# Kernel optimization log

Hardware: AMD Instinct MI355X
Metric: run time of the kernel (lower is better)

The kernel has to match this reference:

```python
import jax, jax.numpy as jnp
import numpy as np

B, S, D_MODEL, N_HEADS = 4, 2048, 1024, 16
HEAD_DIM = D_MODEL // N_HEADS  # 64; used only for the softmax scale, as in the source


def setup_inputs() -> dict:
    key = jax.random.key(0)
    kq, kk, kv, kw = jax.random.split(key, 4)
    q = jax.random.normal(kq, (B, S, D_MODEL), dtype=jnp.float32)
    k = jax.random.normal(kk, (B, S, D_MODEL), dtype=jnp.float32)
    v = jax.random.normal(kv, (B, S, D_MODEL), dtype=jnp.float32)
    # out_proj: nn.Linear(d_model, d_model, bias=False) -> weight [out, in]
    W_out = jax.random.normal(kw, (D_MODEL, D_MODEL), dtype=jnp.float32) * (1.0 / np.sqrt(D_MODEL))
    return {"q": q, "k": k, "v": v, "W_out": W_out}


def reference(q, k, v, W_out):
    scale = 1.0 / jnp.sqrt(jnp.float32(HEAD_DIM))
    # scores: [B, Sq, Sk] -- full quadratic score matrix, as in the source
    scores = jnp.einsum("bqd,bkd->bqk", q, k) * scale
    attn = jax.nn.softmax(scores, axis=-1)
    out = jnp.einsum("bqk,bkd->bqd", attn, v)
    # torch Linear: y = x @ W^T
    return jnp.einsum("bsd,ed->bse", out, W_out)
```

## Files before the change

kernel.cpp:

```cpp
#include <hip/hip_runtime.h>
#include <hip/hip_fp16.h>
#include <stdint.h>

typedef _Float16 h16;
typedef _Float16 h16x8 __attribute__((ext_vector_type(8)));
typedef float f32x4 __attribute__((ext_vector_type(4)));

#define BB 4
#define SS 2048
#define DD 1024

__device__ __forceinline__ void gload16(const void* g, void* l) {
    __builtin_amdgcn_global_load_lds(
        (const __attribute__((address_space(1))) uint32_t*)g,
        (__attribute__((address_space(3))) uint32_t*)l, 16, 0, 0);
}

__global__ __launch_bounds__(256) void cvt_f32_h16(const float* __restrict__ in,
                                                   h16* __restrict__ out,
                                                   int n8, float scale) {
    int i = blockIdx.x * 256 + threadIdx.x;
    if (i >= n8) return;
    const float4* p = (const float4*)in + (size_t)i * 2;
    float4 a = p[0], b = p[1];
    union { int4 i4; h16 h[8]; } u;
    u.h[0] = (h16)(a.x * scale); u.h[1] = (h16)(a.y * scale);
    u.h[2] = (h16)(a.z * scale); u.h[3] = (h16)(a.w * scale);
    u.h[4] = (h16)(b.x * scale); u.h[5] = (h16)(b.y * scale);
    u.h[6] = (h16)(b.z * scale); u.h[7] = (h16)(b.w * scale);
    ((int4*)out)[i] = u.i4;
}

template<int BM, bool F32OUT>
__global__ __launch_bounds__(512, 2) void gemm8p(
    const h16* __restrict__ A, const h16* __restrict__ B, void* __restrict__ Cv,
    int lda, int ldb, int ldc, int K, int tilesN, int tilesMN,
    long long aBatch, long long bBatch, long long cBatch)
{
    constexpr int WROWS  = BM / 2;
    constexpr int MF     = WROWS / 16;
    constexpr int MQ     = MF / 2;
    constexpr int AH     = WROWS / 2;
    constexpr int ALOADS = BM / 128;
    constexpr int ABYTES = BM * 128;
    constexpr int BBYTES = 256 * 128;
    constexpr int BUFB   = ABYTES + BBYTES;

    __shared__ __align__(1024) char lds[2 * BUFB];

    const int tid = threadIdx.x;
    const int nwg = gridDim.x;
    const int bid = blockIdx.x;
    const int wgid = (bid & 7) * (nwg >> 3) + (bid >> 3);
    const int bb  = wgid / tilesMN;
    const int rem = wgid % tilesMN;
    const int tm = rem / tilesN, tn = rem % tilesN;
    const int row0 = tm * BM, col0 = tn * 256;

    const h16* Ab = A + (long long)bb * aBatch;
    const h16* Bb = B + (long long)bb * bBatch;

    const int lane = tid & 63, wid = tid >> 6;
    const int wm = wid >> 2, wn = wid & 3;
    const int frow = lane & 15, kq = lane >> 4;

    const int NT = K >> 6;

    f32x4 acc[MF][4];
#pragma unroll
    for (int m = 0; m < MF; ++m)
#pragma unroll
        for (int n = 0; n < 4; ++n) acc[m][n] = (f32x4){0.f, 0.f, 0.f, 0.f};

    char* l0 = (char*)lds;

    auto STAGE_A = [&](int kt, int buf, int mh) {
#pragma unroll
        for (int i = 0; i < ALOADS; ++i) {
            int d = wid * (ALOADS * 64) + i * 64 + lane;
            int s = d & 7, hr = d >> 3;
            int r = ((hr & ~(AH - 1)) << 1) + mh * AH + (hr & (AH - 1));
            int gg = s ^ (r & 7);
            gload16(Ab + (size_t)(row0 + r) * lda + kt + gg * 8,
                    l0 + buf * BUFB + (r * 8 + s) * 16);
        }
    };
    auto STAGE_B = [&](int kt, int buf, int nh) {
#pragma unroll
        for (int i = 0; i < 2; ++i) {
            int d = wid * 128 + i * 64 + lane;
            int s = d & 7, hr = d >> 3;
            int r = ((hr & ~31) << 1) + nh * 32 + (hr & 31);
            int gg = s ^ (r & 7);
            gload16(Bb + (size_t)(col0 + r) * ldb + kt + gg * 8,
                    l0 + buf * BUFB + ABYTES + (r * 8 + s) * 16);
        }
    };
    auto READ_A = [&](int buf, int mh, h16x8 (&af)[MQ][2]) {
#pragma unroll
        for (int mm = 0; mm < MQ; ++mm)
#pragma unroll
            for (int ks = 0; ks < 2; ++ks) {
                int r = wm * WROWS + (mh * MQ + mm) * 16 + frow;
                int s = (ks * 4 + kq) ^ (r & 7);
                af[mm][ks] = *(const h16x8*)(l0 + buf * BUFB + (r * 8 + s) * 16);
            }
    };
    auto READ_B = [&](int buf, int nh, h16x8 (&bf)[2][2]) {
#pragma unroll
        for (int nn = 0; nn < 2; ++nn)
#pragma unroll
            for (int ks = 0; ks < 2; ++ks) {
                int r = wn * 64 + (nh * 2 + nn) * 16 + frow;
                int s = (ks * 4 + kq) ^ (r & 7);
                bf[nn][ks] = *(const h16x8*)(l0 + buf * BUFB + ABYTES + (r * 8 + s) * 16);
            }
    };
    auto MFMA_Q = [&](int mh, int nh, h16x8 (&af)[MQ][2], h16x8 (&bf)[2][2]) {
        __builtin_amdgcn_s_setprio(1);
#pragma unroll
        for (int ks = 0; ks < 2; ++ks)
#pragma unroll
            for (int mm = 0; mm < MQ; ++mm)
#pragma unroll
                for (int nn = 0; nn < 2; ++nn)
                    acc[mh * MQ + mm][nh * 2 + nn] =
                        __builtin_amdgcn_mfma_f32_16x16x32_f16(
                            af[mm][ks], bf[nn][ks], acc[mh * MQ + mm][nh * 2 + nn], 0, 0, 0);
        __builtin_amdgcn_s_setprio(0);
    };

    STAGE_A(0, 0, 0); STAGE_B(0, 0, 0); STAGE_B(0, 0, 1); STAGE_A(0, 0, 1);
    STAGE_A(64, 1, 0); STAGE_B(64, 1, 0); STAGE_B(64, 1, 1);
    if constexpr (BM == 256) asm volatile("s_waitcnt vmcnt(6)" ::: "memory");
    else                     asm volatile("s_waitcnt vmcnt(5)" ::: "memory");
    __builtin_amdgcn_s_barrier();

    h16x8 af[MQ][2], bf0[2][2], bf1[2][2];

    for (int G = 0; G < NT; ++G) {
        const int buf = G & 1;
        const int kt1 = (G + 1) << 6, kt2 = (G + 2) << 6;
        READ_A(buf, 0, af);
        READ_B(buf, 0, bf0);
        if (G + 1 < NT) STAGE_A(kt1, buf ^ 1, 1);
        __builtin_amdgcn_s_barrier();
        MFMA_Q(0, 0, af, bf0);
        __builtin_amdgcn_s_barrier();
        READ_B(buf, 1, bf1);
        if (G + 2 < NT) STAGE_A(kt2, buf, 0);
        __builtin_amdgcn_s_barrier();
        MFMA_Q(0, 1, af, bf1);
        __builtin_amdgcn_s_barrier();
        READ_A(buf, 1, af);
        if (G + 2 < NT) STAGE_B(kt2, buf, 0);
        __builtin_amdgcn_s_barrier();
        MFMA_Q(1, 0, af, bf0);
        __builtin_amdgcn_s_barrier();
        if (G + 2 < NT) STAGE_B(kt2, buf, 1);
        __builtin_amdgcn_s_barrier();
        MFMA_Q(1, 1, af, bf1);
        if (G + 2 >= NT) {
            asm volatile("s_waitcnt vmcnt(0)" ::: "memory");
        } else if constexpr (BM == 256) {
            asm volatile("s_waitcnt vmcnt(6)" ::: "memory");
        } else {
            asm volatile("s_waitcnt vmcnt(5)" ::: "memory");
        }
        __builtin_amdgcn_s_barrier();
    }

    const int erow = row0 + wm * WROWS + (lane >> 4) * 4;
    const int ecol = col0 + wn * 64 + (lane & 15);
    if (F32OUT) {
        float* C = (float*)Cv + (long long)bb * cBatch;
#pragma unroll
        for (int m = 0; m < MF; ++m)
#pragma unroll
            for (int n = 0; n < 4; ++n)
#pragma unroll
                for (int j = 0; j < 4; ++j)
                    C[(size_t)(erow + m * 16 + j) * ldc + (ecol + n * 16)] = acc[m][n][j];
    } else {
        h16* C = (h16*)Cv + (long long)bb * cBatch;
#pragma unroll
        for (int m = 0; m < MF; ++m)
#pragma unroll
            for (int n = 0; n < 4; ++n)
#pragma unroll
                for (int j = 0; j < 4; ++j)
                    C[(size_t)(erow + m * 16 + j) * ldc + (ecol + n * 16)] = (h16)acc[m][n][j];
    }
}

__global__ __launch_bounds__(256) void softmax_rows(h16* __restrict__ buf) {
    const int row = blockIdx.x;
    h16* rp = buf + (size_t)row * 2048;
    const int t = threadIdx.x;
    const int lane = t & 63, wid = t >> 6;

    union { int4 i4; h16 h[8]; } u;
    u.i4 = ((const int4*)rp)[t];
    float f[8];
#pragma unroll
    for (int j = 0; j < 8; ++j) f[j] = (float)u.h[j];

    float m = f[0];
#pragma unroll
    for (int j = 1; j < 8; ++j) m = fmaxf(m, f[j]);
#pragma unroll
    for (int off = 32; off; off >>= 1) m = fmaxf(m, __shfl_xor(m, off));

    __shared__ float smax[4];
    __shared__ float ssum[4];
    if (lane == 0) smax[wid] = m;
    __syncthreads();
    m = fmaxf(fmaxf(smax[0], smax[1]), fmaxf(smax[2], smax[3]));

    float s = 0.f;
#pragma unroll
    for (int j = 0; j < 8; ++j) { f[j] = __expf(f[j] - m); s += f[j]; }
#pragma unroll
    for (int off = 32; off; off >>= 1) s += __shfl_xor(s, off);
    if (lane == 0) ssum[wid] = s;
    __syncthreads();
    float inv = 1.0f / (ssum[0] + ssum[1] + ssum[2] + ssum[3]);

#pragma unroll
    for (int j = 0; j < 8; ++j) u.h[j] = (h16)(f[j] * inv);
    ((int4*)rp)[t] = u.i4;
}

extern "C" void kernel_launch(void* const* d_in, const int* in_sizes, int n_in,
                              void* d_out, int out_size, void* d_ws, size_t ws_size,
                              hipStream_t stream) {
    (void)in_sizes; (void)n_in; (void)out_size; (void)ws_size;
    const float* q = (const float*)d_in[0];
    const float* k = (const float*)d_in[1];
    const float* v = (const float*)d_in[2];
    const float* w = (const float*)d_in[3];
    float* out = (float*)d_out;

    const size_t QKV = (size_t)BB * SS * DD;
    h16* qh = (h16*)d_ws;
    h16* kh = qh + QKV;
    h16* vh = kh + QKV;
    h16* wh = vh + QKV;
    h16* sc = wh + (size_t)DD * DD;

    cvt_f32_h16<<<(int)(QKV / 8 + 255) / 256, 256, 0, stream>>>(q, qh, (int)(QKV / 8), 0.125f);
    cvt_f32_h16<<<(int)(QKV / 8 + 255) / 256, 256, 0, stream>>>(k, kh, (int)(QKV / 8), 1.0f);
    cvt_f32_h16<<<(int)(QKV / 8 + 255) / 256, 256, 0, stream>>>(v, vh, (int)(QKV / 8), 1.0f);
    cvt_f32_h16<<<(DD * DD / 8 + 255) / 256, 256, 0, stream>>>(w, wh, DD * DD / 8, 1.0f);

    gemm8p<256, false><<<256, 512, 0, stream>>>(
        qh, kh, (void*)sc, DD, DD, SS, DD, 8, 64,
        (long long)SS * DD, (long long)SS * DD, (long long)SS * SS);

    softmax_rows<<<BB * SS, 256, 0, stream>>>(sc);

    h16* vpT = qh;
    gemm8p<128, false><<<256, 512, 0, stream>>>(
        wh, vh, (void*)vpT, DD, DD, BB * SS, DD, 32, 256,
        0LL, 0LL, 0LL);

    gemm8p<128, true><<<256, 512, 0, stream>>>(
        sc, vpT, (void*)out, SS, BB * SS, DD, SS, 4, 64,
        (long long)SS * SS, (long long)SS, (long long)SS * DD);
}
```

Measured before the change: 149.0 us.

## Simplify GEMM pipeline to two-phase schedule and fuse conversion kernels

The four fp32-to-fp16 conversion launches become a single kernel that picks its source by index range, saving launch overhead. The GEMM main loop drops the eight-phase quarter-tile schedule, with a barrier between each quarter, for a two-phase schedule. Each iteration prefetches the whole next K tile up front, then runs two half-tile MFMA blocks that reuse a full set of B fragments, so barriers per iteration fall from seven to two. The cost is less interleaving of loads with MFMAs, more live B fragment registers, and waitcnt values that must exactly match the new load order.

After: 142.1 us. 4.7% less time.

```diff
diff --git a/kernel.cpp b/kernel.cpp
--- a/kernel.cpp
+++ b/kernel.cpp
@@ -16,32 +16,40 @@
         (__attribute__((address_space(3))) uint32_t*)l, 16, 0, 0);
 }
 
-__global__ __launch_bounds__(256) void cvt_f32_h16(const float* __restrict__ in,
-                                                   h16* __restrict__ out,
-                                                   int n8, float scale) {
+__global__ __launch_bounds__(256) void cvt_all(
+    const float* __restrict__ q, const float* __restrict__ k,
+    const float* __restrict__ v, const float* __restrict__ w,
+    h16* __restrict__ qh, h16* __restrict__ kh,
+    h16* __restrict__ vh, h16* __restrict__ wh) {
+    const int NQ = (int)((size_t)BB * SS * DD / 8);
     int i = blockIdx.x * 256 + threadIdx.x;
-    if (i >= n8) return;
-    const float4* p = (const float4*)in + (size_t)i * 2;
+    const float* src; h16* dst; float sc = 1.0f; int j;
+    if (i < NQ)            { src = q; dst = qh; sc = 0.125f; j = i; }
+    else if (i < 2 * NQ)   { src = k; dst = kh; j = i - NQ; }
+    else if (i < 3 * NQ)   { src = v; dst = vh; j = i - 2 * NQ; }
+    else                   { src = w; dst = wh; j = i - 3 * NQ;
+                             if (j >= DD * DD / 8) return; }
+    const float4* p = (const float4*)src + (size_t)j * 2;
     float4 a = p[0], b = p[1];
     union { int4 i4; h16 h[8]; } u;
-    u.h[0] = (h16)(a.x * scale); u.h[1] = (h16)(a.y * scale);
-    u.h[2] = (h16)(a.z * scale); u.h[3] = (h16)(a.w * scale);
-    u.h[4] = (h16)(b.x * scale); u.h[5] = (h16)(b.y * scale);
-    u.h[6] = (h16)(b.z * scale); u.h[7] = (h16)(b.w * scale);
-    ((int4*)out)[i] = u.i4;
+    u.h[0] = (h16)(a.x * sc); u.h[1] = (h16)(a.y * sc);
+    u.h[2] = (h16)(a.z * sc); u.h[3] = (h16)(a.w * sc);
+    u.h[4] = (h16)(b.x * sc); u.h[5] = (h16)(b.y * sc);
+    u.h[6] = (h16)(b.z * sc); u.h[7] = (h16)(b.w * sc);
+    ((int4*)dst)[j] = u.i4;
 }
 
 template<int BM, bool F32OUT>
-__global__ __launch_bounds__(512, 2) void gemm8p(
+__global__ __launch_bounds__(512, 2) void gemm2p(
     const h16* __restrict__ A, const h16* __restrict__ B, void* __restrict__ Cv,
     int lda, int ldb, int ldc, int K, int tilesN, int tilesMN,
     long long aBatch, long long bBatch, long long cBatch)
 {
     constexpr int WROWS  = BM / 2;
     constexpr int MF     = WROWS / 16;
-    constexpr int MQ     = MF / 2;
+    constexpr int MH     = MF / 2;
     constexpr int AH     = WROWS / 2;
-    constexpr int ALOADS = BM / 128;
+    constexpr int AL     = BM / 128;
     constexpr int ABYTES = BM * 128;
     constexpr int BBYTES = 256 * 128;
     constexpr int BUFB   = ABYTES + BBYTES;
@@ -74,10 +82,20 @@
 
     char* l0 = (char*)lds;
 
-    auto STAGE_A = [&](int kt, int buf, int mh) {
-#pragma unroll
-        for (int i = 0; i < ALOADS; ++i) {
-            int d = wid * (ALOADS * 64) + i * 64 + lane;
+    auto STAGE_B = [&](int kt, int buf) {
+#pragma unroll
+        for (int i = 0; i < 4; ++i) {
+            int d = i * 512 + tid;
+            int s = d & 7, r = d >> 3;
+            int gg = s ^ (r & 7);
+            gload16(Bb + (size_t)(col0 + r) * ldb + kt + gg * 8,
+                    l0 + buf * BUFB + ABYTES + (r * 8 + s) * 16);
+        }
+    };
+    auto STAGE_AH = [&](int kt, int buf, int mh) {
+#pragma unroll
+        for (int i = 0; i < AL; ++i) {
+            int d = i * 512 + tid;
             int s = d & 7, hr = d >> 3;
             int r = ((hr & ~(AH - 1)) << 1) + mh * AH + (hr & (AH - 1));
             int gg = s ^ (r & 7);
@@ -85,88 +103,70 @@
                     l0 + buf * BUFB + (r * 8 + s) * 16);
         }
     };
-    auto STAGE_B = [&](int kt, int buf, int nh) {
-#pragma unroll
-        for (int i = 0; i < 2; ++i) {
-            int d = wid * 128 + i * 64 + lane;
-            int s = d & 7, hr = d >> 3;
-            int r = ((hr & ~31) << 1) + nh * 32 + (hr & 31);
-            int gg = s ^ (r & 7);
-            gload16(Bb + (size_t)(col0 + r) * ldb + kt + gg * 8,
-                    l0 + buf * BUFB + ABYTES + (r * 8 + s) * 16);
-        }
-    };
-    auto READ_A = [&](int buf, int mh, h16x8 (&af)[MQ][2]) {
-#pragma unroll
-        for (int mm = 0; mm < MQ; ++mm)
+    auto READ_A = [&](int buf, int mh, h16x8 (&af)[MH][2]) {
+#pragma unroll
+        for (int mm = 0; mm < MH; ++mm)
 #pragma unroll
             for (int ks = 0; ks < 2; ++ks) {
-                int r = wm * WROWS + (mh * MQ + mm) * 16 + frow;
+                int r = wm * WROWS + (mh * MH + mm) * 16 + frow;
                 int s = (ks * 4 + kq) ^ (r & 7);
                 af[mm][ks] = *(const h16x8*)(l0 + buf * BUFB + (r * 8 + s) * 16);
             }
     };
-    auto READ_B = [&](int buf, int nh, h16x8 (&bf)[2][2]) {
-#pragma unroll
-        for (int nn = 0; nn < 2; ++nn)
+    auto READ_B = [&](int buf, h16x8 (&bf)[4][2]) {
+#pragma unroll
+        for (int nn = 0; nn < 4; ++nn)
 #pragma unroll
             for (int ks = 0; ks < 2; ++ks) {
-                int r = wn * 64 + (nh * 2 + nn) * 16 + frow;
+                int r = wn * 64 + nn * 16 + frow;
                 int s = (ks * 4 + kq) ^ (r & 7);
                 bf[nn][ks] = *(const h16x8*)(l0 + buf * BUFB + ABYTES + (r * 8 + s) * 16);
             }
     };
-    auto MFMA_Q = [&](int mh, int nh, h16x8 (&af)[MQ][2], h16x8 (&bf)[2][2]) {
+    auto MFMA_H = [&](int mh, h16x8 (&af)[MH][2], h16x8 (&bf)[4][2]) {
         __builtin_amdgcn_s_setprio(1);
 #pragma unroll
         for (int ks = 0; ks < 2; ++ks)
 #pragma unroll
-            for (int mm = 0; mm < MQ; ++mm)
-#pragma unroll
-                for (int nn = 0; nn < 2; ++nn)
-                    acc[mh * MQ + mm][nh * 2 + nn] =
+            for (int mm = 0; mm < MH; ++mm)
+#pragma unroll
+                for (int nn = 0; nn < 4; ++nn)
+                    acc[mh * MH + mm][nn] =
                         __builtin_amdgcn_mfma_f32_16x16x32_f16(
-                            af[mm][ks], bf[nn][ks], acc[mh * MQ + mm][nh * 2 + nn], 0, 0, 0);
+                            af[mm][ks], bf[nn][ks], acc[mh * MH + mm][nn], 0, 0, 0);
         __builtin_amdgcn_s_setprio(0);
     };
 
-    STAGE_A(0, 0, 0); STAGE_B(0, 0, 0); STAGE_B(0, 0, 1); STAGE_A(0, 0, 1);
-    STAGE_A(64, 1, 0); STAGE_B(64, 1, 0); STAGE_B(64, 1, 1);
-    if constexpr (BM == 256) asm volatile("s_waitcnt vmcnt(6)" ::: "memory");
-    else                     asm volatile("s_waitcnt vmcnt(5)" ::: "memory");
+    STAGE_B(0, 0); STAGE_AH(0, 0, 0); STAGE_AH(0, 0, 1);
+    if constexpr (BM == 256) asm volatile("s_waitcnt vmcnt(2)" ::: "memory");
+    else                     asm volatile("s_waitcnt vmcnt(1)" ::: "memory");
     __builtin_amdgcn_s_barrier();
 
-    h16x8 af[MQ][2], bf0[2][2], bf1[2][2];
+    h16x8 af[MH][2], bf[4][2];
 
     for (int G = 0; G < NT; ++G) {
         const int buf = G & 1;
-        const int kt1 = (G + 1) << 6, kt2 = (G + 2) << 6;
+        const int kt1 = (G + 1) << 6;
+        if (G + 1 < NT) {
+            STAGE_B(kt1, buf ^ 1);
+            STAGE_AH(kt1, buf ^ 1, 0);
+            STAGE_AH(kt1, buf ^ 1, 1);
+        }
         READ_A(buf, 0, af);
-        READ_B(buf, 0, bf0);
-        if (G + 1 < NT) STAGE_A(kt1, buf ^ 1, 1);
-        __builtin_amdgcn_s_barrier();
-        MFMA_Q(0, 0, af, bf0);
-        __builtin_amdgcn_s_barrier();
-        READ_B(buf, 1, bf1);
-        if (G + 2 < NT) STAGE_A(kt2, buf, 0);
-        __builtin_amdgcn_s_barrier();
-        MFMA_Q(0, 1, af, bf1);
+        READ_B(buf, bf);
+        MFMA_H(0, af, bf);
+        if (G + 1 < NT) {
+            if constexpr (BM == 256) asm volatile("s_waitcnt vmcnt(8)" ::: "memory");
+            else                     asm volatile("s_waitcnt vmcnt(6)" ::: "memory");
+        } else {
+            asm volatile("s_waitcnt vmcnt(0)" ::: "memory");
+        }
         __builtin_amdgcn_s_barrier();
         READ_A(buf, 1, af);
-        if (G + 2 < NT) STAGE_B(kt2, buf, 0);
-        __builtin_amdgcn_s_barrier();
-        MFMA_Q(1, 0, af, bf0);
-        __builtin_amdgcn_s_barrier();
-        if (G + 2 < NT) STAGE_B(kt2, buf, 1);
-        __builtin_amdgcn_s_barrier();
-        MFMA_Q(1, 1, af, bf1);
-        if (G + 2 >= NT) {
-            asm volatile("s_waitcnt vmcnt(0)" ::: "memory");
-        } else if constexpr (BM == 256) {
-            asm volatile("s_waitcnt vmcnt(6)" ::: "memory");
-        } else {
-            asm volatile("s_waitcnt vmcnt(5)" ::: "memory");
-        }
+        MFMA_H(1, af, bf);
+        if (G + 1 >= NT) break;
+        if constexpr (BM == 256) asm volatile("s_waitcnt vmcnt(2)" ::: "memory");
+        else                     asm volatile("s_waitcnt vmcnt(1)" ::: "memory");
         __builtin_amdgcn_s_barrier();
     }
 
@@ -248,23 +248,20 @@
     h16* wh = vh + QKV;
     h16* sc = wh + (size_t)DD * DD;
 
-    cvt_f32_h16<<<(int)(QKV / 8 + 255) / 256, 256, 0, stream>>>(q, qh, (int)(QKV / 8), 0.125f);
-    cvt_f32_h16<<<(int)(QKV / 8 + 255) / 256, 256, 0, stream>>>(k, kh, (int)(QKV / 8), 1.0f);
-    cvt_f32_h16<<<(int)(QKV / 8 + 255) / 256, 256, 0, stream>>>(v, vh, (int)(QKV / 8), 1.0f);
-    cvt_f32_h16<<<(DD * DD / 8 + 255) / 256, 256, 0, stream>>>(w, wh, DD * DD / 8, 1.0f);
-
-    gemm8p<256, false><<<256, 512, 0, stream>>>(
+    cvt_all<<<12800, 256, 0, stream>>>(q, k, v, w, qh, kh, vh, wh);
+
+    gemm2p<256, false><<<256, 512, 0, stream>>>(
         qh, kh, (void*)sc, DD, DD, SS, DD, 8, 64,
         (long long)SS * DD, (long long)SS * DD, (long long)SS * SS);
 
     softmax_rows<<<BB * SS, 256, 0, stream>>>(sc);
 
     h16* vpT = qh;
-    gemm8p<128, false><<<256, 512, 0, stream>>>(
+    gemm2p<128, false><<<256, 512, 0, stream>>>(
         wh, vh, (void*)vpT, DD, DD, BB * SS, DD, 32, 256,
         0LL, 0LL, 0LL);
 
-    gemm8p<128, true><<<256, 512, 0, stream>>>(
+    gemm2p<128, true><<<256, 512, 0, stream>>>(
         sc, vpT, (void*)out, SS, BB * SS, DD, SS, 4, 64,
         (long long)SS * SS, (long long)SS, (long long)SS * DD);
 }
```
